# Kernel tuning notes

Hardware: AMD Instinct MI355X
Metric: run time of the kernel (lower is better)

## Reference

```python
import jax, jax.numpy as jnp
import numpy as np


def setup_inputs() -> dict:
    key = jax.random.key(0)
    kx, kf = jax.random.split(key)
    x = jax.random.normal(kx, (1, 3, 512, 512), dtype=jnp.float32)
    # per-pixel 9x9 kernels; normalize each to sum to 1 like a PSF
    kernel_field = jax.random.uniform(kf, (512, 512, 9, 9), dtype=jnp.float32)
    kernel_field = kernel_field / jnp.sum(kernel_field, axis=(-2, -1), keepdims=True)
    return {"x": x, "kernel_field": kernel_field}


def reference(x, kernel_field):
    """Spatially varying blur: out[b,c,h,w] = sum_{i,j} x_pad[b,c,h+i,w+j] * K[h,w,i,j].

    Equivalent to the torch unfold + einsum('bckhw,khw->bchw') but computed as a
    fused shift-multiply-accumulate over the kH*kW offsets, avoiding the
    (B,C,kH*kW,H,W) im2col blowup.
    """
    B, C, H, W = x.shape
    kH, kW = kernel_field.shape[2], kernel_field.shape[3]
    pad = kH // 2
    xp = jnp.pad(x, ((0, 0), (0, 0), (pad, pad), (pad, pad)), mode="reflect")
    out = jnp.zeros_like(x)
    for i in range(kH):          # small fixed loop over kernel taps (81)
        for j in range(kW):
            out = out + xp[:, :, i:i + H, j:j + W] * kernel_field[:, :, i, j]
    return out
```

## Files before the change

kernel.cpp:

```cpp
#include <hip/hip_runtime.h>
#include <stdint.h>

#define H 512
#define W 512
#define HW (H * W)
#define KT 81
#define PAD 4

__device__ __forceinline__ int reflect_idx(int p) {
    if (p < 0) p = -p;
    if (p >= H) p = 2 * H - 2 - p;
    return p;
}

__global__ __launch_bounds__(64) void svblur_kernel(
    const float* __restrict__ x,
    const float* __restrict__ kf,
    float* __restrict__ out)
{
    __shared__ float wlds[64 * KT];

    const int l   = (int)threadIdx.x;
    const int bid = (int)blockIdx.x;
    const int h   = bid >> 3;
    const int w0  = (bid & 7) << 6;

    {
        const float4* ws = (const float4*)(kf + ((size_t)h * W + w0) * KT);
        float4* wd = (float4*)wlds;
#pragma unroll
        for (int it = 0; it < 20; ++it)
            wd[it * 64 + l] = ws[it * 64 + l];
        if (l < 16)
            wd[20 * 64 + l] = ws[20 * 64 + l];
    }

    int rgw[9];
#pragma unroll
    for (int j = 0; j < 9; ++j)
        rgw[j] = reflect_idx(w0 - PAD + l + j);

    const float* wp = wlds + l * KT;
    float a0 = 0.f, a1 = 0.f, a2 = 0.f;

#pragma unroll
    for (int i = 0; i < 9; ++i) {
        const int gh = reflect_idx(h - PAD + i);
        const float* r0 = x + (size_t)gh * W;
        const float* r1 = r0 + HW;
        const float* r2 = r1 + HW;

        float xv0[9], xv1[9], xv2[9];
#pragma unroll
        for (int j = 0; j < 9; ++j) {
            xv0[j] = r0[rgw[j]];
            xv1[j] = r1[rgw[j]];
            xv2[j] = r2[rgw[j]];
        }

#pragma unroll
        for (int j = 0; j < 9; ++j) {
            const float wv = wp[i * 9 + j];
            a0 = fmaf(xv0[j], wv, a0);
            a1 = fmaf(xv1[j], wv, a1);
            a2 = fmaf(xv2[j], wv, a2);
        }
    }

    const int o = h * W + w0 + l;
    out[o]          = a0;
    out[o + HW]     = a1;
    out[o + 2 * HW] = a2;
}

extern "C" void kernel_launch(void* const* d_in, const int* in_sizes, int n_in,
                              void* d_out, int out_size, void* d_ws, size_t ws_size,
                              hipStream_t stream) {
    const float* x  = (const float*)d_in[0];
    const float* kf = (const float*)d_in[1];
    float* out = (float*)d_out;

    dim3 block(64);
    dim3 grid(H * (W / 64));
    svblur_kernel<<<grid, block, 0, stream>>>(x, kf, out);
}
```

Before: 26.66 us.

## Split channels across three wavefronts per block sharing LDS kernel weights

Each block now runs 192 threads, one wavefront per color channel, and all three share the 64-pixel segment's 81-tap weights staged cooperatively in LDS. This raises the wavefront count and spreads the weight staging over more threads. Each thread keeps a single accumulator, which cuts register pressure and per-thread serial work. It adds a __syncthreads barrier, and each channel's weight reads from LDS are now repeated by three wavefronts instead of being reused from registers.

```diff
diff --git a/kernel.cpp b/kernel.cpp
--- a/kernel.cpp
+++ b/kernel.cpp
@@ -6,6 +6,7 @@
 #define HW (H * W)
 #define KT 81
 #define PAD 4
+#define SEGW 64
 
 __device__ __forceinline__ int reflect_idx(int p) {
     if (p < 0) p = -p;
@@ -13,14 +14,16 @@
     return p;
 }
 
-__global__ __launch_bounds__(64) void svblur_kernel(
+__global__ __launch_bounds__(192) void svblur_kernel(
     const float* __restrict__ x,
     const float* __restrict__ kf,
     float* __restrict__ out)
 {
-    __shared__ float wlds[64 * KT];
+    __shared__ float wlds[SEGW * KT];
 
-    const int l   = (int)threadIdx.x;
+    const int tid = (int)threadIdx.x;
+    const int l   = tid & 63;
+    const int wv  = tid >> 6;
     const int bid = (int)blockIdx.x;
     const int h   = bid >> 3;
     const int w0  = (bid & 7) << 6;
@@ -29,48 +32,39 @@
         const float4* ws = (const float4*)(kf + ((size_t)h * W + w0) * KT);
         float4* wd = (float4*)wlds;
 #pragma unroll
-        for (int it = 0; it < 20; ++it)
-            wd[it * 64 + l] = ws[it * 64 + l];
-        if (l < 16)
-            wd[20 * 64 + l] = ws[20 * 64 + l];
+        for (int it = 0; it < 7; ++it) {
+            int idx = (wv * 7 + it) * 64 + l;
+            if (idx < (SEGW * KT) / 4)
+                wd[idx] = ws[idx];
+        }
     }
+    __syncthreads();
 
     int rgw[9];
 #pragma unroll
     for (int j = 0; j < 9; ++j)
         rgw[j] = reflect_idx(w0 - PAD + l + j);
 
+    const float* xc = x + (size_t)wv * HW;
     const float* wp = wlds + l * KT;
-    float a0 = 0.f, a1 = 0.f, a2 = 0.f;
 
+    float acc = 0.f;
 #pragma unroll
     for (int i = 0; i < 9; ++i) {
         const int gh = reflect_idx(h - PAD + i);
-        const float* r0 = x + (size_t)gh * W;
-        const float* r1 = r0 + HW;
-        const float* r2 = r1 + HW;
+        const float* row = xc + (size_t)gh * W;
 
-        float xv0[9], xv1[9], xv2[9];
+        float xv[9];
 #pragma unroll
-        for (int j = 0; j < 9; ++j) {
-            xv0[j] = r0[rgw[j]];
-            xv1[j] = r1[rgw[j]];
-            xv2[j] = r2[rgw[j]];
-        }
+        for (int j = 0; j < 9; ++j)
+            xv[j] = row[rgw[j]];
 
 #pragma unroll
-        for (int j = 0; j < 9; ++j) {
-            const float wv = wp[i * 9 + j];
-            a0 = fmaf(xv0[j], wv, a0);
-            a1 = fmaf(xv1[j], wv, a1);
-            a2 = fmaf(xv2[j], wv, a2);
-        }
+        for (int j = 0; j < 9; ++j)
+            acc = fmaf(xv[j], wp[i * 9 + j], acc);
     }
 
-    const int o = h * W + w0 + l;
-    out[o]          = a0;
-    out[o + HW]     = a1;
-    out[o + 2 * HW] = a2;
+    out[(size_t)wv * HW + h * W + w0 + l] = acc;
 }
 
 extern "C" void kernel_launch(void* const* d_in, const int* in_sizes, int n_in,
@@ -80,7 +74,7 @@
     const float* kf = (const float*)d_in[1];
     float* out = (float*)d_out;
 
-    dim3 block(64);
-    dim3 grid(H * (W / 64));
+    dim3 block(192);
+    dim3 grid(H * (W / SEGW));
     svblur_kernel<<<grid, block, 0, stream>>>(x, kf, out);
 }
```

Result: faster. 24.24 us (-9.1%).
